# Optimization experiments

Hardware: AMD Instinct MI355X
Metric: run time of the kernel (lower is better)

Reference implementation:

```python
import jax, jax.numpy as jnp
import numpy as np

N, E, G = 2048, 65536, 32
F_ATOM, LAT, IN, ED, NB, L = 16, 64, 128, 32, 5, 5


def setup_inputs() -> dict:
    key = jax.random.key(0)
    ks = iter(jax.random.split(key, 64))
    nxt = lambda: next(ks)
    def w(shape):
        fan_in = shape[-2] if len(shape) >= 2 else 1
        return jax.random.normal(nxt(), shape, jnp.float32) / np.sqrt(fan_in)
    inp = {}
    inp['x'] = jax.random.normal(nxt(), (N, F_ATOM), jnp.float32)
    inp['t'] = jax.random.uniform(nxt(), (G, 1), jnp.float32)
    inp['z'] = jax.random.normal(nxt(), (N, LAT), jnp.float32)
    inp['edge_index'] = jax.random.randint(nxt(), (2, E), 0, N, jnp.int32)
    inp['edge_attr'] = jax.random.normal(nxt(), (E, NB), jnp.float32)
    inp['batch'] = jnp.sort(jax.random.randint(nxt(), (N,), 0, G, jnp.int32))
    inp['batch_edge_global'] = jax.random.randint(nxt(), (E,), 0, G, jnp.int32)
    # top-level dense layers
    inp['Wt_a'] = w((1, IN)); inp['bt_a'] = jnp.zeros((IN,))
    inp['Wt_b'] = w((1, ED)); inp['bt_b'] = jnp.zeros((ED,))
    inp['W_atom'] = w((F_ATOM, IN)); inp['b_atom'] = jnp.zeros((IN,))
    inp['W_bond'] = w((NB, ED)); inp['b_bond'] = jnp.zeros((ED,))
    inp['W_lat'] = w((LAT, IN)); inp['b_lat'] = jnp.zeros((IN,))
    inp['W_at'] = w((IN, IN)); inp['b_at'] = jnp.zeros((IN,))
    inp['W_bt'] = w((ED, ED)); inp['b_bt'] = jnp.zeros((ED,))
    # TopoEdgeGNN: L layers of edge-conditioned message passing with edge update
    inp['Wmsg'] = w((L, 2 * IN + ED, IN)); inp['bmsg'] = jnp.zeros((L, IN))
    inp['Wnode'] = w((L, 2 * IN, IN)); inp['bnode'] = jnp.zeros((L, IN))
    inp['Wedge'] = w((L, 2 * IN + ED, ED)); inp['bedge'] = jnp.zeros((L, ED))
    # prediction head
    inp['Wsh'] = w((IN, IN)); inp['bsh'] = jnp.zeros((IN,))
    inp['Wbm'] = w((ED, IN)); inp['bbm'] = jnp.zeros((IN,))
    inp['Wbl'] = w((IN, NB)); inp['bbl'] = jnp.zeros((NB,))
    inp['Wal'] = w((IN, F_ATOM + LAT)); inp['bal'] = jnp.zeros((F_ATOM + LAT,))
    return inp


def reference(x, t, z, edge_index, edge_attr, batch, batch_edge_global,
              Wt_a, bt_a, Wt_b, bt_b, W_atom, b_atom, W_bond, b_bond,
              W_lat, b_lat, W_at, b_at, W_bt, b_bt,
              Wmsg, bmsg, Wnode, bnode, Wedge, bedge,
              Wsh, bsh, Wbm, bbm, Wbl, bbl, Wal, bal):
    j, i = edge_index[0], edge_index[1]
    # time embeddings, gathered to nodes / edges
    ta = t @ Wt_a + bt_a            # [G, IN]
    tb = t @ Wt_b + bt_b            # [G, ED]
    tnode = ta[batch]               # [N, IN]
    tedge = tb[batch_edge_global]   # [E, ED]
    # node features
    s = x @ W_atom + b_atom
    s = (s + tnode) @ W_at + b_at
    s = s + (z @ W_lat + b_lat)
    # edge features
    e = edge_attr @ W_bond + b_bond
    e = (e + tedge) @ W_bt + b_bt
    # TopoEdgeGNN: message passing with residual node/edge updates
    for l in range(L):
        m = jax.nn.silu(jnp.concatenate([s[i], s[j], e], -1) @ Wmsg[l] + bmsg[l])  # [E, IN]
        agg = jax.ops.segment_sum(m, i, num_segments=N)                            # [N, IN]
        s = s + jax.nn.silu(jnp.concatenate([s, agg], -1) @ Wnode[l] + bnode[l])
        e = e + jax.nn.silu(jnp.concatenate([s[i], s[j], e], -1) @ Wedge[l] + bedge[l])
    # prediction head
    s2 = jax.nn.silu(s @ Wsh + bsh)
    al = s2 @ Wal + bal
    atoms_pred, latent_pred = al[:, :F_ATOM], al[:, F_ATOM:]
    # dense edge symmetrization: scatter edges into [N, N, ED], symmetrize, gather back
    e_dense = jnp.zeros((N, N, ED), e.dtype).at[j, i].set(e)
    e_dense = 0.5 * (e_dense + e_dense.transpose(1, 0, 2))
    e_sym = e_dense[j, i]           # [E, ED]
    f = jax.nn.silu(s2[i] + s2[j] + (e_sym @ Wbm + bbm))
    bonds_pred = f @ Wbl + bbl
    return latent_pred, atoms_pred, bonds_pred
```

## Files before the change

### kernel.cpp

```cpp
#include <hip/hip_runtime.h>
#include <hip/hip_bf16.h>

#define NN 2048
#define NE 65536
#define NG 32
#define CIN 128
#define CED 32
#define CLAT 64
#define CFA 16
#define CNB 5
#define NL 5

#define OFF_AT (NN * CLAT)
#define OFF_B  (NN * CLAT + NN * CFA)

typedef __attribute__((ext_vector_type(8))) short bf16x8;
typedef __attribute__((ext_vector_type(4))) float f32x4;

__device__ __forceinline__ float silu_f(float v) { return v / (1.0f + __expf(-v)); }
__device__ __forceinline__ short f2bs(float v) {
    __hip_bfloat16 h = __float2bfloat16(v);
    return *reinterpret_cast<short*>(&h);
}
__device__ __forceinline__ float bs2f(short s) {
    return __bfloat162float(*reinterpret_cast<__hip_bfloat16*>(&s));
}
__device__ __forceinline__ unsigned pack2(float a, float b) {
    return ((unsigned)(unsigned short)f2bs(b) << 16) | (unsigned short)f2bs(a);
}

struct KArgs {
    const float *x, *t, *z;
    const int *jj, *ii;
    const float *ea;
    const int *batch, *beg;
    const float *Wt_a, *bt_a, *Wt_b, *bt_b, *W_atom, *b_atom, *W_bond, *b_bond;
    const float *W_lat, *b_lat, *W_at, *b_at, *W_bt, *b_bt;
    const float *Wmsg, *bmsg, *Wnode, *bnode, *Wedge, *bedge;
    const float *Wsh, *bsh, *Wbm, *bbm, *Wbl, *bbl, *Wal, *bal;
    float *s, *e, *agg;
    int *cnt, *rowpos, *invp, *i_s, *j_s;
    float *s2, *U, *V, *P, *Q;
    int *map;
    short *s_bf, *e_bf;
    short *Wpn, *Wpsh, *Wpal, *Wpbm, *Wproj, *W3m, *We3;
    float *out;
};

__device__ __forceinline__ void phase_pack(const KArgs& a, int start, int stride)
{
    for (int idx = start; idx < 6 * 4 * 20 * 64 * 8; idx += stride) {
        int j = idx & 7, t0 = idx >> 3, lane = t0 & 63, tt = t0 >> 6;
        int kq = (lane >> 4) * 8 + j, n16 = lane & 15;
        if (idx < NL * 8 * 8 * 64 * 8) {
            int nt = tt & 7, kt = (tt >> 3) & 7, l = tt >> 6;
            a.Wpn[idx] = f2bs(a.Wnode[((size_t)l * 256 + kt * 32 + kq) * CIN + nt * 16 + n16]);
        }
        if (idx < 4 * 8 * 64 * 8) {
            int nt = tt & 7, kt = tt >> 3;
            a.Wpsh[idx] = f2bs(a.Wsh[(size_t)(kt * 32 + kq) * CIN + nt * 16 + n16]);
        }
        if (idx < 4 * 5 * 64 * 8) {
            int nt = tt % 5, kt = tt / 5;
            a.Wpal[idx] = f2bs(a.Wal[(size_t)(kt * 32 + kq) * 80 + nt * 16 + n16]);
        }
        if (idx < 8 * 64 * 8) {
            int nt = tt & 7;
            a.Wpbm[idx] = f2bs(a.Wbm[(size_t)kq * CIN + nt * 16 + n16]);
        }
        {
            int nt = tt % 20; int t2 = tt / 20; int kt = t2 & 3; int slot = t2 >> 2;
            int k = kt * 32 + kq;
            float v;
            if (nt < 16) {
                int msgl = slot % 5;
                int srcK = (nt < 8) ? k : 128 + k;
                int col = (nt & 7) * 16 + n16;
                v = a.Wmsg[((size_t)msgl * 288 + srcK) * CIN + col];
            } else {
                int edgel = (slot == 0) ? 0 : slot - 1;
                int srcK = (nt < 18) ? k : 128 + k;
                int col = (nt & 1) * 16 + n16;
                v = a.Wedge[((size_t)edgel * 288 + srcK) * CED + col];
            }
            a.Wproj[idx] = f2bs(v);
        }
        if (idx < NL * 8 * 64 * 8) {
            int nt = tt & 7, l = tt >> 3;
            a.W3m[idx] = f2bs(a.Wmsg[((size_t)l * 288 + 256 + kq) * CIN + nt * 16 + n16]);
        }
        if (idx < NL * 2 * 64 * 8) {
            int nt = tt & 1, l = tt >> 1;
            a.We3[idx] = f2bs(a.Wedge[((size_t)l * 288 + 256 + kq) * CED + nt * 16 + n16]);
        }
    }
}

__device__ __forceinline__ void phase_init_s(const KArgs& a, char* smem, int tile, int tid)
{
    float* xs  = (float*)smem;
    float* zs  = (float*)(smem + 1024);
    float* tmp = (float*)(smem + 5120);
    float* tv  = (float*)(smem + 13312);
    int nb0 = tile * 16;
    int c = tid & 127, h = tid >> 7;
    if (tid < 16 * CFA / 4) ((float4*)xs)[tid] = ((const float4*)a.x)[nb0 * (CFA / 4) + tid];
    if (tid < 16 * CLAT / 4) ((float4*)zs)[tid] = ((const float4*)a.z)[nb0 * (CLAT / 4) + tid];
    if (tid < 16) tv[tid] = a.t[a.batch[nb0 + tid]];
    __syncthreads();
    float wta = a.Wt_a[c], base0 = a.b_atom[c] + a.bt_a[c];
    float acc[8];
#pragma unroll
    for (int q = 0; q < 8; q++) acc[q] = base0 + tv[h * 8 + q] * wta;
    for (int k = 0; k < CFA; k++) {
        float w = a.W_atom[k * CIN + c];
#pragma unroll
        for (int q = 0; q < 8; q++) acc[q] += xs[(h * 8 + q) * CFA + k] * w;
    }
#pragma unroll
    for (int q = 0; q < 8; q++) tmp[(h * 8 + q) * CIN + c] = acc[q];
    __syncthreads();
    float base1 = a.b_at[c] + a.b_lat[c];
    float acc2[8];
#pragma unroll
    for (int q = 0; q < 8; q++) acc2[q] = base1;
    for (int k4 = 0; k4 < CIN / 4; k4++) {
        float w0 = a.W_at[(4 * k4 + 0) * CIN + c], w1 = a.W_at[(4 * k4 + 1) * CIN + c];
        float w2 = a.W_at[(4 * k4 + 2) * CIN + c], w3 = a.W_at[(4 * k4 + 3) * CIN + c];
#pragma unroll
        for (int q = 0; q < 8; q++) {
            float4 f = *(const float4*)&tmp[(h * 8 + q) * CIN + 4 * k4];
            acc2[q] += f.x * w0 + f.y * w1 + f.z * w2 + f.w * w3;
        }
    }
    for (int k4 = 0; k4 < CLAT / 4; k4++) {
        float w0 = a.W_lat[(4 * k4 + 0) * CIN + c], w1 = a.W_lat[(4 * k4 + 1) * CIN + c];
        float w2 = a.W_lat[(4 * k4 + 2) * CIN + c], w3 = a.W_lat[(4 * k4 + 3) * CIN + c];
#pragma unroll
        for (int q = 0; q < 8; q++) {
            float4 f = *(const float4*)&zs[(h * 8 + q) * CLAT + 4 * k4];
            acc2[q] += f.x * w0 + f.y * w1 + f.z * w2 + f.w * w3;
        }
    }
#pragma unroll
    for (int q = 0; q < 8; q++) {
        int nd = nb0 + h * 8 + q;
        a.s[(size_t)nd * CIN + c] = acc2[q];
        a.s_bf[(size_t)nd * CIN + c] = f2bs(acc2[q]);
    }
}

__device__ __forceinline__ void phase_init_e(const KArgs& a, char* smem, int tb, int tid)
{
    float* eas   = (float*)smem;
    float* tv    = (float*)(smem + 1280);
    int*   sp    = (int*)(smem + 1536);
    float* tmp   = (float*)(smem + 1792);
    float* wbt   = (float*)(smem + 10240);
    float* wbond = (float*)(smem + 14336);
    float* cb    = (float*)(smem + 14976);
    float* wtb   = (float*)(smem + 15104);
    float* bbt2  = (float*)(smem + 15232);
    int k0 = tb * 64;
    for (int idx = tid; idx < 320; idx += 256) eas[idx] = a.ea[(size_t)k0 * 5 + idx];
    if (tid < 64) { tv[tid] = a.t[a.beg[k0 + tid]]; sp[tid] = a.invp[k0 + tid]; }
    for (int idx = tid; idx < 1024; idx += 256) wbt[idx] = a.W_bt[idx];
    if (tid < 160) wbond[tid] = a.W_bond[tid];
    if (tid < 32) { cb[tid] = a.b_bond[tid] + a.bt_b[tid]; wtb[tid] = a.Wt_b[tid]; bbt2[tid] = a.b_bt[tid]; }
    __syncthreads();
    int ch = tid & 31, eg = tid >> 5;
#pragma unroll
    for (int q = 0; q < 8; q++) {
        int le = eg * 8 + q;
        float acc = cb[ch] + tv[le] * wtb[ch];
#pragma unroll
        for (int bb = 0; bb < CNB; bb++) acc += eas[le * 5 + bb] * wbond[bb * 32 + ch];
        tmp[le * 33 + ch] = acc;
    }
    __syncthreads();
#pragma unroll
    for (int q = 0; q < 8; q++) {
        int le = eg * 8 + q;
        float acc2 = bbt2[ch];
        for (int d = 0; d < 32; d++) acc2 += tmp[le * 33 + d] * wbt[d * 32 + ch];
        size_t ix = (size_t)sp[le] * CED + ch;
        a.e[ix] = acc2;
        a.e_bf[ix] = f2bs(acc2);
        if (ch == 0) {
            int k = k0 + le;
            atomicMax(&a.map[(size_t)a.jj[k] * NN + a.ii[k]], k);
        }
    }
}

__device__ __forceinline__ void phase_node_proj(
    const KArgs& a, char* smem, int tile, int tid, bool DO_NODE, bool DO_POST,
    const short* Wpn_l, const float* bnode_l, const short* Wproj_slot)
{
    short* feat  = (short*)smem;
    short* feat2 = (short*)(smem + 8448);
    int nb0 = tile * 16;
    int lane = tid & 63, w = tid >> 6;
    int quad = lane >> 4, n16 = lane & 15;

    if (DO_NODE) {
        { int kl = tid >> 4, c = tid & 15;
          *(uint4*)&feat[kl * 264 + c * 8] = ((const uint4*)a.s_bf)[(size_t)(nb0 + kl) * 16 + c]; }
        for (int idx = tid; idx < 16 * 32; idx += 256) {
            int kl = idx >> 5, c = idx & 31;
            size_t gix = (size_t)(nb0 + kl) * 32 + c;
            float4 v = ((const float4*)a.agg)[gix];
            ((float4*)a.agg)[gix] = (float4){0.f, 0.f, 0.f, 0.f};
            uint2 p; p.x = pack2(v.x, v.y); p.y = pack2(v.z, v.w);
            *(uint2*)&feat[kl * 264 + 128 + 4 * c] = p;
        }
        __syncthreads();
        f32x4 acc[2];
        acc[0] = (f32x4){0.f, 0.f, 0.f, 0.f};
        acc[1] = (f32x4){0.f, 0.f, 0.f, 0.f};
        const short* fbase = feat + n16 * 264 + quad * 8;
#pragma unroll
        for (int kt = 0; kt < 8; kt++) {
            bf16x8 av = *(const bf16x8*)(fbase + kt * 32);
#pragma unroll
            for (int n2 = 0; n2 < 2; n2++) {
                int nt = w * 2 + n2;
                bf16x8 b = *(const bf16x8*)(Wpn_l + ((size_t)(kt * 8 + nt) * 64 + lane) * 8);
                acc[n2] = __builtin_amdgcn_mfma_f32_16x16x32_bf16(av, b, acc[n2], 0, 0, 0);
            }
        }
#pragma unroll
        for (int n2 = 0; n2 < 2; n2++) {
            int col = (w * 2 + n2) * 16 + n16;
            float bb = bnode_l[col];
#pragma unroll
            for (int r = 0; r < 4; r++) {
                int row = quad * 4 + r;
                size_t ix = (size_t)(nb0 + row) * CIN + col;
                float v = a.s[ix] + silu_f(acc[n2][r] + bb);
                a.s[ix] = v;
                short bv = f2bs(v);
                a.s_bf[ix] = bv;
                feat2[row * 136 + col] = bv;
            }
        }
        __syncthreads();
    } else {
        int kl = tid >> 4, c = tid & 15;
        *(uint4*)&feat2[kl * 136 + c * 8] = ((const uint4*)a.s_bf)[(size_t)(nb0 + kl) * 16 + c];
        __syncthreads();
    }

    {
        f32x4 accp[5];
#pragma unroll
        for (int t2 = 0; t2 < 5; t2++) accp[t2] = (f32x4){0.f, 0.f, 0.f, 0.f};
        const short* abase = feat2 + n16 * 136 + quad * 8;
#pragma unroll
        for (int kt = 0; kt < 4; kt++) {
            bf16x8 av = *(const bf16x8*)(abase + kt * 32);
#pragma unroll
            for (int n5 = 0; n5 < 5; n5++) {
                int nt = w * 5 + n5;
                bf16x8 b = *(const bf16x8*)(Wproj_slot + ((size_t)(kt * 20 + nt) * 64 + lane) * 8);
                accp[n5] = __builtin_amdgcn_mfma_f32_16x16x32_bf16(av, b, accp[n5], 0, 0, 0);
            }
        }
#pragma unroll
        for (int n5 = 0; n5 < 5; n5++) {
            int nt = w * 5 + n5;
#pragma unroll
            for (int r = 0; r < 4; r++) {
                int node = tile * 16 + quad * 4 + r;
                float v = accp[n5][r];
                if (nt < 8)       a.U[(size_t)node * CIN + nt * 16 + n16] = v;
                else if (nt < 16) a.V[(size_t)node * CIN + (nt - 8) * 16 + n16] = v;
                else if (nt < 18) a.P[(size_t)node * CED + (nt - 16) * 16 + n16] = v;
                else              a.Q[(size_t)node * CED + (nt - 18) * 16 + n16] = v;
            }
        }
    }

    if (DO_POST) {
        short* feat_s2 = feat;
        const short* fbase = feat2 + n16 * 136 + quad * 8;
        f32x4 acc[2];
        acc[0] = (f32x4){0.f, 0.f, 0.f, 0.f};
        acc[1] = (f32x4){0.f, 0.f, 0.f, 0.f};
#pragma unroll
        for (int kt = 0; kt < 4; kt++) {
            bf16x8 av = *(const bf16x8*)(fbase + kt * 32);
#pragma unroll
            for (int n2 = 0; n2 < 2; n2++) {
                int nt = w * 2 + n2;
                bf16x8 b = *(const bf16x8*)(a.Wpsh + ((size_t)(kt * 8 + nt) * 64 + lane) * 8);
                acc[n2] = __builtin_amdgcn_mfma_f32_16x16x32_bf16(av, b, acc[n2], 0, 0, 0);
            }
        }
#pragma unroll
        for (int n2 = 0; n2 < 2; n2++) {
            int col = (w * 2 + n2) * 16 + n16;
            float bb = a.bsh[col];
#pragma unroll
            for (int r = 0; r < 4; r++) {
                int row = quad * 4 + r;
                float v = silu_f(acc[n2][r] + bb);
                a.s2[(size_t)(nb0 + row) * CIN + col] = v;
                feat_s2[row * 136 + col] = f2bs(v);
            }
        }
        __syncthreads();
        const short* abase2 = feat_s2 + n16 * 136 + quad * 8;
        f32x4 acca[2];
        acca[0] = (f32x4){0.f, 0.f, 0.f, 0.f};
        acca[1] = (f32x4){0.f, 0.f, 0.f, 0.f};
        int nAl = (w == 0) ? 2 : 1;
        int ntl[2] = {w, 4};
#pragma unroll
        for (int kt = 0; kt < 4; kt++) {
            bf16x8 av = *(const bf16x8*)(abase2 + kt * 32);
#pragma unroll
            for (int q = 0; q < 2; q++) {
                if (q < nAl) {
                    bf16x8 b = *(const bf16x8*)(a.Wpal + ((size_t)(kt * 5 + ntl[q]) * 64 + lane) * 8);
                    acca[q] = __builtin_amdgcn_mfma_f32_16x16x32_bf16(av, b, acca[q], 0, 0, 0);
                }
            }
        }
#pragma unroll
        for (int q = 0; q < 2; q++) {
            if (q < nAl) {
                int col = ntl[q] * 16 + n16;
                float bb = a.bal[col];
#pragma unroll
                for (int r = 0; r < 4; r++) {
                    int node = nb0 + quad * 4 + r;
                    float v = acca[q][r] + bb;
                    if (col < CFA) a.out[OFF_AT + node * CFA + col] = v;
                    else           a.out[(size_t)node * CLAT + (col - CFA)] = v;
                }
            }
        }
    }
}

__device__ __forceinline__ void phase_em(
    const KArgs& a, char* smem, int tb, int tid, bool DO_EDGE, bool DO_MSG,
    const short* We3p, const float* bedge_l, const short* W3mp, const float* bmsg_l)
{
    short* feat_e = (short*)smem;
    short* uv_bf  = (short*)(smem + 5120);
    short* pq_bf  = (short*)(smem + 22528);
    int*   sii    = (int*)(smem + 27648);
    int*   sjj    = (int*)(smem + 27904);
    int e0 = tb * 64;
    if (tid < 64) sii[tid] = a.i_s[e0 + tid];
    else if (tid < 128) sjj[tid - 64] = a.j_s[e0 + tid - 64];
    __syncthreads();
    { int kl = tid >> 2, c = tid & 3;
      uint4 v = ((const uint4*)a.e_bf)[(size_t)e0 * 4 + tid];
      *(uint4*)&feat_e[kl * 40 + c * 8] = v; }
    if (DO_EDGE) {
        for (int idx = tid; idx < 64 * 8; idx += 256) {
            int kl = idx >> 3, c = idx & 7;
            float4 av = ((const float4*)a.P)[(size_t)sii[kl] * 8 + c];
            float4 bv = ((const float4*)a.Q)[(size_t)sjj[kl] * 8 + c];
            uint2 p; p.x = pack2(av.x + bv.x, av.y + bv.y); p.y = pack2(av.z + bv.z, av.w + bv.w);
            *(uint2*)&pq_bf[kl * 40 + 4 * c] = p;
        }
    }
    if (DO_MSG) {
        for (int idx = tid; idx < 64 * 32; idx += 256) {
            int kl = idx >> 5, c = idx & 31;
            float4 av = ((const float4*)a.U)[(size_t)sii[kl] * 32 + c];
            float4 bv = ((const float4*)a.V)[(size_t)sjj[kl] * 32 + c];
            uint2 p; p.x = pack2(av.x + bv.x, av.y + bv.y); p.y = pack2(av.z + bv.z, av.w + bv.w);
            *(uint2*)&uv_bf[kl * 136 + 4 * c] = p;
        }
    }
    __syncthreads();
    int lane = tid & 63, w = tid >> 6;
    int quad = lane >> 4, n16 = lane & 15;
    const short* abase = feat_e + (w * 16 + n16) * 40 + quad * 8;
    bf16x8 av = *(const bf16x8*)abase;

    if (DO_EDGE) {
        f32x4 acc_e[2];
        acc_e[0] = (f32x4){0.f, 0.f, 0.f, 0.f};
        acc_e[1] = (f32x4){0.f, 0.f, 0.f, 0.f};
#pragma unroll
        for (int nt = 0; nt < 2; nt++) {
            bf16x8 b = *(const bf16x8*)(We3p + ((size_t)(nt * 64 + lane)) * 8);
            acc_e[nt] = __builtin_amdgcn_mfma_f32_16x16x32_bf16(av, b, acc_e[nt], 0, 0, 0);
        }
#pragma unroll
        for (int nt = 0; nt < 2; nt++) {
            int ch = nt * 16 + n16;
            float bb = bedge_l[ch];
#pragma unroll
            for (int r = 0; r < 4; r++) {
                int el = w * 16 + quad * 4 + r;
                size_t ix = (size_t)(e0 + el) * CED + ch;
                float v = a.e[ix] + silu_f(acc_e[nt][r] + bb + bs2f(pq_bf[el * 40 + ch]));
                a.e[ix] = v;
                short bv = f2bs(v);
                a.e_bf[ix] = bv;
                feat_e[el * 40 + ch] = bv;
            }
        }
        av = *(const bf16x8*)abase;
    }

    if (DO_MSG) {
        f32x4 acc_m[8];
#pragma unroll
        for (int t2 = 0; t2 < 8; t2++) acc_m[t2] = (f32x4){0.f, 0.f, 0.f, 0.f};
#pragma unroll
        for (int nt = 0; nt < 8; nt++) {
            bf16x8 b = *(const bf16x8*)(W3mp + ((size_t)(nt * 64 + lane)) * 8);
            acc_m[nt] = __builtin_amdgcn_mfma_f32_16x16x32_bf16(av, b, acc_m[nt], 0, 0, 0);
        }
#pragma unroll
        for (int nt = 0; nt < 8; nt++) {
            int ch = nt * 16 + n16;
            float bb = bmsg_l[ch];
#pragma unroll
            for (int r = 0; r < 4; r++) {
                int el = w * 16 + quad * 4 + r;
                int lix = el * 136 + ch;
                float m = silu_f(acc_m[nt][r] + bb + bs2f(uv_bf[lix]));
                uv_bf[lix] = f2bs(m);
            }
        }
        __syncthreads();
        if (tid < 128) {
            int c = tid;
            float run = 0.f;
            int cur = sii[0];
            for (int r = 0; r < 64; r++) {
                int tg = sii[r];
                if (tg != cur) { atomicAdd(&a.agg[(size_t)cur * CIN + c], run); run = 0.f; cur = tg; }
                run += bs2f(uv_bf[r * 136 + c]);
            }
            atomicAdd(&a.agg[(size_t)cur * CIN + c], run);
        }
    }
}

__device__ __forceinline__ void phase_post_edge(const KArgs& a, char* smem, int tb, int tid)
{
    short* esym  = (short*)smem;
    float* sbias = (float*)(smem + 5120);
    int* sii = (int*)(smem + 38912);
    int* sjj = (int*)(smem + 39168);
    int* skf = (int*)(smem + 39424);
    int* skb = (int*)(smem + 39680);
    int e0 = tb * 64;
    if (tid < 64) sii[tid] = a.ii[e0 + tid];
    else if (tid < 128) sjj[tid - 64] = a.jj[e0 + tid - 64];
    __syncthreads();
    if (tid < 64) skf[tid] = a.invp[a.map[(size_t)sjj[tid] * NN + sii[tid]]];
    else if (tid < 128) {
        int m = a.map[(size_t)sii[tid - 64] * NN + sjj[tid - 64]];
        skb[tid - 64] = (m >= 0) ? a.invp[m] : -1;
    }
    __syncthreads();
    for (int idx = tid; idx < 64 * 8; idx += 256) {
        int kl = idx >> 3, c = idx & 7;
        float4 av = ((const float4*)a.e)[(size_t)skf[kl] * 8 + c];
        int kb = skb[kl];
        float4 bv = {0.f, 0.f, 0.f, 0.f};
        if (kb >= 0) bv = ((const float4*)a.e)[(size_t)kb * 8 + c];
        uint2 p; p.x = pack2(0.5f * (av.x + bv.x), 0.5f * (av.y + bv.y));
        p.y = pack2(0.5f * (av.z + bv.z), 0.5f * (av.w + bv.w));
        *(uint2*)&esym[kl * 40 + 4 * c] = p;
    }
    for (int idx = tid; idx < 64 * 32; idx += 256) {
        int kl = idx >> 5, c = idx & 31;
        float4 av = ((const float4*)a.s2)[(size_t)sii[kl] * 32 + c];
        float4 bv = ((const float4*)a.s2)[(size_t)sjj[kl] * 32 + c];
        *(float4*)&sbias[kl * 132 + 4 * c] = (float4){av.x + bv.x, av.y + bv.y, av.z + bv.z, av.w + bv.w};
    }
    __syncthreads();
    int lane = tid & 63, w = tid >> 6;
    int quad = lane >> 4, n16 = lane & 15;
    bf16x8 av = *(const bf16x8*)(esym + (w * 16 + n16) * 40 + quad * 8);
    f32x4 acc[8];
#pragma unroll
    for (int nt = 0; nt < 8; nt++) {
        bf16x8 b = *(const bf16x8*)(a.Wpbm + ((size_t)nt * 64 + lane) * 8);
        f32x4 zero = {0.f, 0.f, 0.f, 0.f};
        acc[nt] = __builtin_amdgcn_mfma_f32_16x16x32_bf16(av, b, zero, 0, 0, 0);
    }
    float f[8][4];
#pragma unroll
    for (int nt = 0; nt < 8; nt++) {
        int col = nt * 16 + n16;
        float bb = a.bbm[col];
#pragma unroll
        for (int r = 0; r < 4; r++) {
            int row = w * 16 + quad * 4 + r;
            f[nt][r] = silu_f(acc[nt][r] + bb + sbias[row * 132 + col]);
        }
    }
    __syncthreads();
    float* fshT = sbias;
#pragma unroll
    for (int nt = 0; nt < 8; nt++) {
        int col = nt * 16 + n16;
#pragma unroll
        for (int r = 0; r < 4; r++) {
            int row = w * 16 + quad * 4 + r;
            fshT[col * 66 + row] = f[nt][r];
        }
    }
    __syncthreads();
    for (int idx = tid; idx < 64 * CNB; idx += 256) {
        int kl = idx / CNB, b = idx - kl * CNB;
        float acc3 = a.bbl[b];
        for (int d = 0; d < CIN; d++) acc3 += fshT[d * 66 + kl] * a.Wbl[d * CNB + b];
        a.out[OFF_B + (size_t)(e0 + kl) * CNB + b] = acc3;
    }
}

__global__ __launch_bounds__(256) void k_prologue(KArgs a)
{
    __shared__ __align__(16) char smem[13440];
    int b = blockIdx.x, tid = threadIdx.x;
    if (b < 960) phase_pack(a, b * 256 + tid, 960 * 256);
    else if (b < 1088) phase_init_s(a, smem, b - 960, tid);
    else {
        int base = (b - 1088) * 1024;
#pragma unroll
        for (int q = 0; q < 4; q++) atomicAdd(&a.cnt[a.ii[base + q * 256 + tid]], 1);
    }
}
__global__ __launch_bounds__(256) void k_prefix(KArgs a)
{
    __shared__ int part[256];
    int tid = threadIdx.x;
    int loc[8], sum = 0;
#pragma unroll
    for (int q = 0; q < 8; q++) { loc[q] = a.cnt[tid * 8 + q]; sum += loc[q]; }
    part[tid] = sum;
    __syncthreads();
    if (tid == 0) { int r = 0; for (int i = 0; i < 256; i++) { int v = part[i]; part[i] = r; r += v; } }
    __syncthreads();
    int r = part[tid];
#pragma unroll
    for (int q = 0; q < 8; q++) { a.rowpos[tid * 8 + q] = r; r += loc[q]; }
}
__global__ void k_perm(KArgs a)
{
    int k = blockIdx.x * 256 + threadIdx.x;
    int iv = a.ii[k];
    int p = atomicAdd(&a.rowpos[iv], 1);
    a.invp[k] = p;
    a.i_s[p] = iv;
    a.j_s[p] = a.jj[k];
}
__global__ __launch_bounds__(256) void k_init_e(KArgs a)
{
    __shared__ __align__(16) char smem[15360];
    phase_init_e(a, smem, blockIdx.x, threadIdx.x);
}
__global__ __launch_bounds__(256) void k_node_proj(KArgs a, int donode, int dopost,
                                                   const short* Wpn_l, const float* bnode_l,
                                                   const short* Wproj_slot)
{
    __shared__ __align__(16) char smem[12800];
    phase_node_proj(a, smem, blockIdx.x, threadIdx.x, donode != 0, dopost != 0,
                    Wpn_l, bnode_l, Wproj_slot);
}
__global__ __launch_bounds__(256) void k_em(KArgs a, int de, int dm, const short* We3p,
                                            const float* bedge_l, const short* W3mp, const float* bmsg_l)
{
    __shared__ __align__(16) char smem[28160];
    phase_em(a, smem, blockIdx.x, threadIdx.x, de != 0, dm != 0, We3p, bedge_l, W3mp, bmsg_l);
}
__global__ __launch_bounds__(256) void k_post_edge(KArgs a)
{
    __shared__ __align__(16) char smem[39936];
    phase_post_edge(a, smem, blockIdx.x, threadIdx.x);
}

extern "C" void kernel_launch(void* const* d_in, const int* in_sizes, int n_in,
                              void* d_out, int out_size, void* d_ws, size_t ws_size,
                              hipStream_t stream) {
    KArgs a;
    a.x      = (const float*)d_in[0];
    a.t      = (const float*)d_in[1];
    a.z      = (const float*)d_in[2];
    const int* eidx = (const int*)d_in[3];
    a.jj     = eidx;
    a.ii     = eidx + NE;
    a.ea     = (const float*)d_in[4];
    a.batch  = (const int*)d_in[5];
    a.beg    = (const int*)d_in[6];
    a.Wt_a   = (const float*)d_in[7];
    a.bt_a   = (const float*)d_in[8];
    a.Wt_b   = (const float*)d_in[9];
    a.bt_b   = (const float*)d_in[10];
    a.W_atom = (const float*)d_in[11];
    a.b_atom = (const float*)d_in[12];
    a.W_bond = (const float*)d_in[13];
    a.b_bond = (const float*)d_in[14];
    a.W_lat  = (const float*)d_in[15];
    a.b_lat  = (const float*)d_in[16];
    a.W_at   = (const float*)d_in[17];
    a.b_at   = (const float*)d_in[18];
    a.W_bt   = (const float*)d_in[19];
    a.b_bt   = (const float*)d_in[20];
    a.Wmsg   = (const float*)d_in[21];
    a.bmsg   = (const float*)d_in[22];
    a.Wnode  = (const float*)d_in[23];
    a.bnode  = (const float*)d_in[24];
    a.Wedge  = (const float*)d_in[25];
    a.bedge  = (const float*)d_in[26];
    a.Wsh    = (const float*)d_in[27];
    a.bsh    = (const float*)d_in[28];
    a.Wbm    = (const float*)d_in[29];
    a.bbm    = (const float*)d_in[30];
    a.Wbl    = (const float*)d_in[31];
    a.bbl    = (const float*)d_in[32];
    a.Wal    = (const float*)d_in[33];
    a.bal    = (const float*)d_in[34];

    a.s      = (float*)d_ws;
    a.e      = a.s + (size_t)NN * CIN;
    a.agg    = a.e + (size_t)NE * CED;
    a.cnt    = (int*)(a.agg + (size_t)NN * CIN);
    a.rowpos = a.cnt + NN;
    a.invp   = a.rowpos + NN;
    a.i_s    = a.invp + NE;
    a.j_s    = a.i_s + NE;
    a.s2     = (float*)(a.j_s + NE);
    a.U      = a.s2 + (size_t)NN * CIN;
    a.V      = a.U + (size_t)NN * CIN;
    a.P      = a.V + (size_t)NN * CIN;
    a.Q      = a.P + (size_t)NN * CED;
    a.map    = (int*)(a.Q + (size_t)NN * CED);
    a.s_bf   = (short*)(a.map + (size_t)NN * NN);
    a.e_bf   = a.s_bf + (size_t)NN * CIN;
    a.Wpn    = a.e_bf + (size_t)NE * CED;
    a.Wpsh   = a.Wpn + (size_t)NL * 8 * 8 * 64 * 8;
    a.Wpal   = a.Wpsh + (size_t)4 * 8 * 64 * 8;
    a.Wpbm   = a.Wpal + (size_t)4 * 5 * 64 * 8;
    a.Wproj  = a.Wpbm + (size_t)8 * 64 * 8;
    a.W3m    = a.Wproj + (size_t)6 * 4 * 20 * 64 * 8;
    a.We3    = a.W3m + (size_t)NL * 8 * 64 * 8;
    a.out    = (float*)d_out;

    hipMemsetAsync(a.map, 0xFF, (size_t)NN * NN * sizeof(int), stream);
    hipMemsetAsync(a.agg, 0, ((size_t)NN * CIN + NN) * sizeof(float), stream);

    k_prologue<<<1152, 256, 0, stream>>>(a);
    k_prefix<<<1, 256, 0, stream>>>(a);
    k_perm<<<NE / 256, 256, 0, stream>>>(a);
    k_init_e<<<NE / 64, 256, 0, stream>>>(a);
    k_node_proj<<<NN / 16, 256, 0, stream>>>(a, 0, 0, nullptr, nullptr, a.Wproj);
    k_em<<<NE / 64, 256, 0, stream>>>(a, 0, 1, nullptr, nullptr, a.W3m, a.bmsg);
    for (int l = 0; l < NL; l++) {
        int dopost = (l == NL - 1) ? 1 : 0;
        k_node_proj<<<NN / 16, 256, 0, stream>>>(a, 1, dopost,
            a.Wpn + (size_t)l * 8 * 8 * 64 * 8, a.bnode + l * CIN,
            a.Wproj + (size_t)(l + 1) * 4 * 20 * 64 * 8);
        int dm = (l < NL - 1) ? 1 : 0;
        k_em<<<NE / 64, 256, 0, stream>>>(a, 1, dm,
            a.We3 + (size_t)l * 2 * 64 * 8, a.bedge + l * CED,
            dm ? a.W3m + (size_t)(l + 1) * 8 * 64 * 8 : a.W3m,
            dm ? a.bmsg + (l + 1) * CIN : a.bmsg);
    }
    k_post_edge<<<NE / 64, 256, 0, stream>>>(a);
}
```

Measured before the change: 358.6 us.

## Fuse all phases into one persistent kernel with software grid barriers

Replaces the sequence of about sixteen kernel launches and two memsets with a single persistent kernel of 1024 blocks. The phases are separated by atomic-based grid barriers, and the fused path is used only when occupancy allows all blocks to be co-resident. Node and edge state are kept in registers across layers instead of round-tripping through global memory, and the bf16 shadow copies of s and e are dropped. The post-edge shared buffers also move to bf16 to cut LDS use. The aim is to remove launch gaps and redundant global traffic, at the cost of barrier spin overhead and some extra precision loss in the bias path.

```diff
diff --git a/kernel.cpp b/kernel.cpp
--- a/kernel.cpp
+++ b/kernel.cpp
@@ -42,10 +42,28 @@
     int *cnt, *rowpos, *invp, *i_s, *j_s;
     float *s2, *U, *V, *P, *Q;
     int *map;
-    short *s_bf, *e_bf;
     short *Wpn, *Wpsh, *Wpal, *Wpbm, *Wproj, *W3m, *We3;
+    int *gsync;
     float *out;
 };
+
+__device__ __forceinline__ void gbar(int* bar, int* gen, int nb)
+{
+    __threadfence();
+    __syncthreads();
+    if (threadIdx.x == 0) {
+        int g = __hip_atomic_load(gen, __ATOMIC_RELAXED, __HIP_MEMORY_SCOPE_AGENT);
+        if (__hip_atomic_fetch_add(bar, 1, __ATOMIC_ACQ_REL, __HIP_MEMORY_SCOPE_AGENT) == nb - 1) {
+            __hip_atomic_store(bar, 0, __ATOMIC_RELAXED, __HIP_MEMORY_SCOPE_AGENT);
+            __hip_atomic_store(gen, g + 1, __ATOMIC_RELEASE, __HIP_MEMORY_SCOPE_AGENT);
+        } else {
+            while (__hip_atomic_load(gen, __ATOMIC_ACQUIRE, __HIP_MEMORY_SCOPE_AGENT) == g)
+                __builtin_amdgcn_s_sleep(2);
+        }
+    }
+    __syncthreads();
+    __threadfence();
+}
 
 __device__ __forceinline__ void phase_pack(const KArgs& a, int start, int stride)
 {
@@ -146,7 +164,6 @@
     for (int q = 0; q < 8; q++) {
         int nd = nb0 + h * 8 + q;
         a.s[(size_t)nd * CIN + c] = acc2[q];
-        a.s_bf[(size_t)nd * CIN + c] = f2bs(acc2[q]);
     }
 }
 
@@ -185,7 +202,6 @@
         for (int d = 0; d < 32; d++) acc2 += tmp[le * 33 + d] * wbt[d * 32 + ch];
         size_t ix = (size_t)sp[le] * CED + ch;
         a.e[ix] = acc2;
-        a.e_bf[ix] = f2bs(acc2);
         if (ch == 0) {
             int k = k0 + le;
             atomicMax(&a.map[(size_t)a.jj[k] * NN + a.ii[k]], k);
@@ -193,9 +209,10 @@
     }
 }
 
-__device__ __forceinline__ void phase_node_proj(
+__device__ __forceinline__ void phase_node2(
     const KArgs& a, char* smem, int tile, int tid, bool DO_NODE, bool DO_POST,
-    const short* Wpn_l, const float* bnode_l, const short* Wproj_slot)
+    bool LOAD_S, bool STORE_S,
+    const short* Wpn_l, const float* bnode_l, const short* Wproj_slot, float (*s_reg)[4])
 {
     short* feat  = (short*)smem;
     short* feat2 = (short*)(smem + 8448);
@@ -204,8 +221,16 @@
     int quad = lane >> 4, n16 = lane & 15;
 
     if (DO_NODE) {
-        { int kl = tid >> 4, c = tid & 15;
-          *(uint4*)&feat[kl * 264 + c * 8] = ((const uint4*)a.s_bf)[(size_t)(nb0 + kl) * 16 + c]; }
+#pragma unroll
+        for (int n2 = 0; n2 < 2; n2++) {
+            int col = (w * 2 + n2) * 16 + n16;
+#pragma unroll
+            for (int r = 0; r < 4; r++) {
+                int row = quad * 4 + r;
+                if (LOAD_S) s_reg[n2][r] = a.s[(size_t)(nb0 + row) * CIN + col];
+                feat[row * 264 + col] = f2bs(s_reg[n2][r]);
+            }
+        }
         for (int idx = tid; idx < 16 * 32; idx += 256) {
             int kl = idx >> 5, c = idx & 31;
             size_t gix = (size_t)(nb0 + kl) * 32 + c;
@@ -236,18 +261,20 @@
 #pragma unroll
             for (int r = 0; r < 4; r++) {
                 int row = quad * 4 + r;
-                size_t ix = (size_t)(nb0 + row) * CIN + col;
-                float v = a.s[ix] + silu_f(acc[n2][r] + bb);
-                a.s[ix] = v;
-                short bv = f2bs(v);
-                a.s_bf[ix] = bv;
-                feat2[row * 136 + col] = bv;
+                float v = s_reg[n2][r] + silu_f(acc[n2][r] + bb);
+                s_reg[n2][r] = v;
+                if (STORE_S) a.s[(size_t)(nb0 + row) * CIN + col] = v;
+                feat2[row * 136 + col] = f2bs(v);
             }
         }
         __syncthreads();
     } else {
         int kl = tid >> 4, c = tid & 15;
-        *(uint4*)&feat2[kl * 136 + c * 8] = ((const uint4*)a.s_bf)[(size_t)(nb0 + kl) * 16 + c];
+        const float4* sp4 = (const float4*)&a.s[(size_t)(nb0 + kl) * CIN + c * 8];
+        float4 v0 = sp4[0], v1 = sp4[1];
+        uint4 p; p.x = pack2(v0.x, v0.y); p.y = pack2(v0.z, v0.w);
+        p.z = pack2(v1.x, v1.y); p.w = pack2(v1.z, v1.w);
+        *(uint4*)&feat2[kl * 136 + c * 8] = p;
         __syncthreads();
     }
 
@@ -344,9 +371,10 @@
     }
 }
 
-__device__ __forceinline__ void phase_em(
-    const KArgs& a, char* smem, int tb, int tid, bool DO_EDGE, bool DO_MSG,
-    const short* We3p, const float* bedge_l, const short* W3mp, const float* bmsg_l)
+__device__ __forceinline__ void phase_em2(
+    const KArgs& a, char* smem, int tb, int tid, bool DO_EDGE, bool DO_MSG, bool LOAD_E, bool WRITE_E,
+    const short* We3p, const float* bedge_l, const short* W3mp, const float* bmsg_l,
+    float (*e_reg)[4])
 {
     short* feat_e = (short*)smem;
     short* uv_bf  = (short*)(smem + 5120);
@@ -354,12 +382,21 @@
     int*   sii    = (int*)(smem + 27648);
     int*   sjj    = (int*)(smem + 27904);
     int e0 = tb * 64;
+    int lane = tid & 63, w = tid >> 6;
+    int quad = lane >> 4, n16 = lane & 15;
     if (tid < 64) sii[tid] = a.i_s[e0 + tid];
     else if (tid < 128) sjj[tid - 64] = a.j_s[e0 + tid - 64];
     __syncthreads();
-    { int kl = tid >> 2, c = tid & 3;
-      uint4 v = ((const uint4*)a.e_bf)[(size_t)e0 * 4 + tid];
-      *(uint4*)&feat_e[kl * 40 + c * 8] = v; }
+#pragma unroll
+    for (int nt = 0; nt < 2; nt++) {
+        int ch = nt * 16 + n16;
+#pragma unroll
+        for (int r = 0; r < 4; r++) {
+            int el = w * 16 + quad * 4 + r;
+            if (LOAD_E) e_reg[nt][r] = a.e[(size_t)(e0 + el) * CED + ch];
+            feat_e[el * 40 + ch] = f2bs(e_reg[nt][r]);
+        }
+    }
     if (DO_EDGE) {
         for (int idx = tid; idx < 64 * 8; idx += 256) {
             int kl = idx >> 3, c = idx & 7;
@@ -379,8 +416,6 @@
         }
     }
     __syncthreads();
-    int lane = tid & 63, w = tid >> 6;
-    int quad = lane >> 4, n16 = lane & 15;
     const short* abase = feat_e + (w * 16 + n16) * 40 + quad * 8;
     bf16x8 av = *(const bf16x8*)abase;
 
@@ -400,12 +435,10 @@
 #pragma unroll
             for (int r = 0; r < 4; r++) {
                 int el = w * 16 + quad * 4 + r;
-                size_t ix = (size_t)(e0 + el) * CED + ch;
-                float v = a.e[ix] + silu_f(acc_e[nt][r] + bb + bs2f(pq_bf[el * 40 + ch]));
-                a.e[ix] = v;
-                short bv = f2bs(v);
-                a.e_bf[ix] = bv;
-                feat_e[el * 40 + ch] = bv;
+                float v = e_reg[nt][r] + silu_f(acc_e[nt][r] + bb + bs2f(pq_bf[el * 40 + ch]));
+                e_reg[nt][r] = v;
+                feat_e[el * 40 + ch] = f2bs(v);
+                if (WRITE_E) a.e[(size_t)(e0 + el) * CED + ch] = v;
             }
         }
         av = *(const bf16x8*)abase;
@@ -450,11 +483,11 @@
 __device__ __forceinline__ void phase_post_edge(const KArgs& a, char* smem, int tb, int tid)
 {
     short* esym  = (short*)smem;
-    float* sbias = (float*)(smem + 5120);
-    int* sii = (int*)(smem + 38912);
-    int* sjj = (int*)(smem + 39168);
-    int* skf = (int*)(smem + 39424);
-    int* skb = (int*)(smem + 39680);
+    short* sbias = (short*)(smem + 5120);
+    int* sii = (int*)(smem + 22016);
+    int* sjj = (int*)(smem + 22272);
+    int* skf = (int*)(smem + 22528);
+    int* skb = (int*)(smem + 22784);
     int e0 = tb * 64;
     if (tid < 64) sii[tid] = a.ii[e0 + tid];
     else if (tid < 128) sjj[tid - 64] = a.jj[e0 + tid - 64];
@@ -479,7 +512,8 @@
         int kl = idx >> 5, c = idx & 31;
         float4 av = ((const float4*)a.s2)[(size_t)sii[kl] * 32 + c];
         float4 bv = ((const float4*)a.s2)[(size_t)sjj[kl] * 32 + c];
-        *(float4*)&sbias[kl * 132 + 4 * c] = (float4){av.x + bv.x, av.y + bv.y, av.z + bv.z, av.w + bv.w};
+        uint2 p; p.x = pack2(av.x + bv.x, av.y + bv.y); p.y = pack2(av.z + bv.z, av.w + bv.w);
+        *(uint2*)&sbias[kl * 132 + 4 * c] = p;
     }
     __syncthreads();
     int lane = tid & 63, w = tid >> 6;
@@ -500,27 +534,102 @@
 #pragma unroll
         for (int r = 0; r < 4; r++) {
             int row = w * 16 + quad * 4 + r;
-            f[nt][r] = silu_f(acc[nt][r] + bb + sbias[row * 132 + col]);
-        }
-    }
-    __syncthreads();
-    float* fshT = sbias;
+            f[nt][r] = silu_f(acc[nt][r] + bb + bs2f(sbias[row * 132 + col]));
+        }
+    }
+    __syncthreads();
+    short* fshT = sbias;
 #pragma unroll
     for (int nt = 0; nt < 8; nt++) {
         int col = nt * 16 + n16;
 #pragma unroll
         for (int r = 0; r < 4; r++) {
             int row = w * 16 + quad * 4 + r;
-            fshT[col * 66 + row] = f[nt][r];
+            fshT[col * 66 + row] = f2bs(f[nt][r]);
         }
     }
     __syncthreads();
     for (int idx = tid; idx < 64 * CNB; idx += 256) {
         int kl = idx / CNB, b = idx - kl * CNB;
         float acc3 = a.bbl[b];
-        for (int d = 0; d < CIN; d++) acc3 += fshT[d * 66 + kl] * a.Wbl[d * CNB + b];
+        for (int d = 0; d < CIN; d++) acc3 += bs2f(fshT[d * 66 + kl]) * a.Wbl[d * CNB + b];
         a.out[OFF_B + (size_t)(e0 + kl) * CNB + b] = acc3;
     }
+}
+
+__global__ __launch_bounds__(256, 4) void k_main(KArgs a)
+{
+    __shared__ __align__(16) char smem[28160];
+    int bid = blockIdx.x, tid = threadIdx.x;
+    int* bar = a.gsync; int* gen = a.gsync + 1;
+
+    a.agg[bid * 256 + tid] = 0.f;
+    if (bid < 8) a.cnt[bid * 256 + tid] = 0;
+    gbar(bar, gen, 1024);
+
+    if (bid < 128) phase_init_s(a, smem, bid, tid);
+    else phase_pack(a, (bid - 128) * 256 + tid, 896 * 256);
+    if (bid >= 192 && bid < 448) atomicAdd(&a.cnt[a.ii[(bid - 192) * 256 + tid]], 1);
+    {
+        int4 m1 = {-1, -1, -1, -1};
+#pragma unroll
+        for (int q = 0; q < 4; q++)
+            ((int4*)a.map)[(size_t)bid * 1024 + q * 256 + tid] = m1;
+    }
+    gbar(bar, gen, 1024);
+
+    if (bid == 0) {
+        int* part = (int*)smem;
+        int loc[8], sum = 0;
+#pragma unroll
+        for (int q = 0; q < 8; q++) { loc[q] = a.cnt[tid * 8 + q]; sum += loc[q]; }
+        part[tid] = sum;
+        __syncthreads();
+        if (tid == 0) { int r = 0; for (int i = 0; i < 256; i++) { int v = part[i]; part[i] = r; r += v; } }
+        __syncthreads();
+        int r = part[tid];
+#pragma unroll
+        for (int q = 0; q < 8; q++) { a.rowpos[tid * 8 + q] = r; r += loc[q]; }
+    }
+    gbar(bar, gen, 1024);
+
+    if (bid < 256) {
+        int k = bid * 256 + tid;
+        int iv = a.ii[k];
+        int p = atomicAdd(&a.rowpos[iv], 1);
+        a.invp[k] = p;
+        a.i_s[p] = iv;
+        a.j_s[p] = a.jj[k];
+    }
+    gbar(bar, gen, 1024);
+
+    phase_init_e(a, smem, bid, tid);
+    gbar(bar, gen, 1024);
+
+    float s_reg[2][4], e_reg[2][4];
+
+    if (bid < 128) phase_node2(a, smem, bid, tid, false, false, false, false,
+                               nullptr, nullptr, a.Wproj, s_reg);
+    gbar(bar, gen, 1024);
+
+    phase_em2(a, smem, bid, tid, false, true, true, false, nullptr, nullptr, a.W3m, a.bmsg, e_reg);
+    gbar(bar, gen, 1024);
+
+    for (int l = 0; l < NL; l++) {
+        if (bid < 128)
+            phase_node2(a, smem, bid, tid, true, l == NL - 1, l == 0, false,
+                        a.Wpn + (size_t)l * 8 * 8 * 64 * 8, a.bnode + l * CIN,
+                        a.Wproj + (size_t)(l + 1) * 4 * 20 * 64 * 8, s_reg);
+        gbar(bar, gen, 1024);
+        bool dm = (l < NL - 1);
+        phase_em2(a, smem, bid, tid, true, dm, false, l == NL - 1,
+                  a.We3 + (size_t)l * 2 * 64 * 8, a.bedge + l * CED,
+                  dm ? a.W3m + (size_t)(l + 1) * 8 * 64 * 8 : a.W3m,
+                  dm ? a.bmsg + (l + 1) * CIN : a.bmsg, e_reg);
+        gbar(bar, gen, 1024);
+    }
+
+    phase_post_edge(a, smem, bid, tid);
 }
 
 __global__ __launch_bounds__(256) void k_prologue(KArgs a)
@@ -569,18 +678,21 @@
                                                    const short* Wproj_slot)
 {
     __shared__ __align__(16) char smem[12800];
-    phase_node_proj(a, smem, blockIdx.x, threadIdx.x, donode != 0, dopost != 0,
-                    Wpn_l, bnode_l, Wproj_slot);
+    float s_reg[2][4];
+    phase_node2(a, smem, blockIdx.x, threadIdx.x, donode != 0, dopost != 0,
+                donode != 0, donode != 0, Wpn_l, bnode_l, Wproj_slot, s_reg);
 }
 __global__ __launch_bounds__(256) void k_em(KArgs a, int de, int dm, const short* We3p,
                                             const float* bedge_l, const short* W3mp, const float* bmsg_l)
 {
     __shared__ __align__(16) char smem[28160];
-    phase_em(a, smem, blockIdx.x, threadIdx.x, de != 0, dm != 0, We3p, bedge_l, W3mp, bmsg_l);
+    float e_reg[2][4];
+    phase_em2(a, smem, blockIdx.x, threadIdx.x, de != 0, dm != 0, true, de != 0,
+              We3p, bedge_l, W3mp, bmsg_l, e_reg);
 }
 __global__ __launch_bounds__(256) void k_post_edge(KArgs a)
 {
-    __shared__ __align__(16) char smem[39936];
+    __shared__ __align__(16) char smem[23040];
     phase_post_edge(a, smem, blockIdx.x, threadIdx.x);
 }
 
@@ -640,36 +752,51 @@
     a.P      = a.V + (size_t)NN * CIN;
     a.Q      = a.P + (size_t)NN * CED;
     a.map    = (int*)(a.Q + (size_t)NN * CED);
-    a.s_bf   = (short*)(a.map + (size_t)NN * NN);
-    a.e_bf   = a.s_bf + (size_t)NN * CIN;
-    a.Wpn    = a.e_bf + (size_t)NE * CED;
+    a.Wpn    = (short*)(a.map + (size_t)NN * NN);
     a.Wpsh   = a.Wpn + (size_t)NL * 8 * 8 * 64 * 8;
     a.Wpal   = a.Wpsh + (size_t)4 * 8 * 64 * 8;
     a.Wpbm   = a.Wpal + (size_t)4 * 5 * 64 * 8;
     a.Wproj  = a.Wpbm + (size_t)8 * 64 * 8;
     a.W3m    = a.Wproj + (size_t)6 * 4 * 20 * 64 * 8;
     a.We3    = a.W3m + (size_t)NL * 8 * 64 * 8;
+    a.gsync  = (int*)(a.We3 + (size_t)NL * 2 * 64 * 8);
     a.out    = (float*)d_out;
 
-    hipMemsetAsync(a.map, 0xFF, (size_t)NN * NN * sizeof(int), stream);
-    hipMemsetAsync(a.agg, 0, ((size_t)NN * CIN + NN) * sizeof(float), stream);
-
-    k_prologue<<<1152, 256, 0, stream>>>(a);
-    k_prefix<<<1, 256, 0, stream>>>(a);
-    k_perm<<<NE / 256, 256, 0, stream>>>(a);
-    k_init_e<<<NE / 64, 256, 0, stream>>>(a);
-    k_node_proj<<<NN / 16, 256, 0, stream>>>(a, 0, 0, nullptr, nullptr, a.Wproj);
-    k_em<<<NE / 64, 256, 0, stream>>>(a, 0, 1, nullptr, nullptr, a.W3m, a.bmsg);
-    for (int l = 0; l < NL; l++) {
-        int dopost = (l == NL - 1) ? 1 : 0;
-        k_node_proj<<<NN / 16, 256, 0, stream>>>(a, 1, dopost,
-            a.Wpn + (size_t)l * 8 * 8 * 64 * 8, a.bnode + l * CIN,
-            a.Wproj + (size_t)(l + 1) * 4 * 20 * 64 * 8);
-        int dm = (l < NL - 1) ? 1 : 0;
-        k_em<<<NE / 64, 256, 0, stream>>>(a, 1, dm,
-            a.We3 + (size_t)l * 2 * 64 * 8, a.bedge + l * CED,
-            dm ? a.W3m + (size_t)(l + 1) * 8 * 64 * 8 : a.W3m,
-            dm ? a.bmsg + (l + 1) * CIN : a.bmsg);
-    }
-    k_post_edge<<<NE / 64, 256, 0, stream>>>(a);
-}
+    static int use_fused = -1;
+    if (use_fused < 0) {
+        int dev = 0;
+        (void)hipGetDevice(&dev);
+        hipDeviceProp_t props;
+        int ncu = 0;
+        if (hipGetDeviceProperties(&props, dev) == hipSuccess) ncu = props.multiProcessorCount;
+        int maxb = 0;
+        if (hipOccupancyMaxActiveBlocksPerMultiprocessor(&maxb, k_main, 256, 0) != hipSuccess) maxb = 0;
+        use_fused = ((long)maxb * ncu >= 1024) ? 1 : 0;
+    }
+
+    if (use_fused) {
+        hipMemsetAsync(a.gsync, 0, 2 * sizeof(int), stream);
+        k_main<<<1024, 256, 0, stream>>>(a);
+    } else {
+        hipMemsetAsync(a.map, 0xFF, (size_t)NN * NN * sizeof(int), stream);
+        hipMemsetAsync(a.agg, 0, ((size_t)NN * CIN + NN) * sizeof(float), stream);
+        k_prologue<<<1152, 256, 0, stream>>>(a);
+        k_prefix<<<1, 256, 0, stream>>>(a);
+        k_perm<<<NE / 256, 256, 0, stream>>>(a);
+        k_init_e<<<NE / 64, 256, 0, stream>>>(a);
+        k_node_proj<<<NN / 16, 256, 0, stream>>>(a, 0, 0, nullptr, nullptr, a.Wproj);
+        k_em<<<NE / 64, 256, 0, stream>>>(a, 0, 1, nullptr, nullptr, a.W3m, a.bmsg);
+        for (int l = 0; l < NL; l++) {
+            int dopost = (l == NL - 1) ? 1 : 0;
+            k_node_proj<<<NN / 16, 256, 0, stream>>>(a, 1, dopost,
+                a.Wpn + (size_t)l * 8 * 8 * 64 * 8, a.bnode + l * CIN,
+                a.Wproj + (size_t)(l + 1) * 4 * 20 * 64 * 8);
+            int dm = (l < NL - 1) ? 1 : 0;
+            k_em<<<NE / 64, 256, 0, stream>>>(a, 1, dm,
+                a.We3 + (size_t)l * 2 * 64 * 8, a.bedge + l * CED,
+                dm ? a.W3m + (size_t)(l + 1) * 8 * 64 * 8 : a.W3m,
+                dm ? a.bmsg + (l + 1) * CIN : a.bmsg);
+        }
+        k_post_edge<<<NE / 64, 256, 0, stream>>>(a);
+    }
+}
```

After: 355.7 us. Within noise of the previous version (-0.8%).
